# Kernel tuning notes

Measured on AMD Instinct MI355X. Metric: run time of the kernel, lower is better.

The kernel has to match this reference:

```python
import jax, jax.numpy as jnp
import numpy as np

E_DIM = 1024
HID = 4096
H = (2 * HID) // 3  # floor(2*hidden/3) = 2730
NUM_EXPERTS = 8
TOP_K = 2
LN_EPS = 1e-5


def setup_inputs() -> dict:
    key = jax.random.key(0)
    ks = jax.random.split(key, 10)
    B, T, P = 2, 8, 256
    s_in = 1.0 / np.sqrt(E_DIM)
    s_h = 1.0 / np.sqrt(H)
    return {
        "x": jax.random.normal(ks[0], (B, T, P, E_DIM), jnp.float32),
        "Wr": jax.random.normal(ks[1], (NUM_EXPERTS, E_DIM), jnp.float32) * s_in,
        "Wv": jax.random.normal(ks[2], (NUM_EXPERTS, E_DIM, H), jnp.float32) * s_in,
        "bv": jax.random.normal(ks[3], (NUM_EXPERTS, H), jnp.float32) * 0.01,
        "Wg": jax.random.normal(ks[4], (NUM_EXPERTS, E_DIM, H), jnp.float32) * s_in,
        "bg": jax.random.normal(ks[5], (NUM_EXPERTS, H), jnp.float32) * 0.01,
        "Wo": jax.random.normal(ks[6], (NUM_EXPERTS, H, E_DIM), jnp.float32) * s_h,
        "bo": jax.random.normal(ks[7], (NUM_EXPERTS, E_DIM), jnp.float32) * 0.01,
        "ln_g": jnp.ones((E_DIM,), jnp.float32),
        "ln_b": jnp.zeros((E_DIM,), jnp.float32),
    }


def reference(x, Wr, Wv, bv, Wg, bg, Wo, bo, ln_g, ln_b):
    B, T, P, E = x.shape
    flat = x.reshape(-1, E)          # [N, E]
    N = flat.shape[0]

    # router: top-k logits -> softmax combine weights
    logits = flat @ Wr.T                              # [N, C]
    tk_vals, tk_idx = jax.lax.top_k(logits, TOP_K)    # [N, K]
    tk_w = jax.nn.softmax(tk_vals, axis=-1)           # [N, K]

    # dense combine-weight matrix: zero for non-routed experts
    comb = jnp.zeros((N, NUM_EXPERTS), flat.dtype)
    comb = comb.at[jnp.arange(N)[:, None], tk_idx].add(tk_w)  # [N, C]

    # all experts over all tokens (masked combine makes this exact)
    hv = jnp.einsum('ne,ceh->cnh', flat, Wv) + bv[:, None, :]  # [C, N, H]
    hg = jnp.einsum('ne,ceh->cnh', flat, Wg) + bg[:, None, :]
    h = jax.nn.silu(hv) * hg                                   # SwiGLU
    oe = jnp.einsum('cnh,che->cne', h, Wo) + bo[:, None, :]    # [C, N, E]
    out = jnp.einsum('cne,nc->ne', oe, comb)                   # weighted combine

    # residual + LayerNorm (AdaptiveNormalizer with no conditioning)
    y = x + out.reshape(B, T, P, E)
    mu = jnp.mean(y, axis=-1, keepdims=True)
    var = jnp.mean((y - mu) ** 2, axis=-1, keepdims=True)
    return ln_g * (y - mu) * jax.lax.rsqrt(var + LN_EPS) + ln_b
```

## Files before the change

kernel.cpp:

```cpp
#include <hip/hip_runtime.h>
#include <hip/hip_bf16.h>

#define E_DIM 1024
#define HDIM  2730
#define HP    2752
#define NEXP  8
#define NTOK  4096
#define NPAIR 8192
#define LN_EPS 1e-5f

typedef __attribute__((ext_vector_type(8))) short  short8;
typedef __attribute__((ext_vector_type(4))) float  floatx4;
typedef __attribute__((ext_vector_type(4))) int    intx4;

__device__ __forceinline__ __hip_bfloat16 f2bf(float f) { return __float2bfloat16(f); }

__global__ __launch_bounds__(256) void router_k(const float* __restrict__ x,
    const float* __restrict__ Wr, int* __restrict__ counts,
    int* __restrict__ tk_idx, float* __restrict__ tk_w) {
  int wid = threadIdx.x >> 6, lane = threadIdx.x & 63;
  int t = blockIdx.x * 4 + wid;
  const float* xr = x + (size_t)t * E_DIM;
  float xv[16];
#pragma unroll
  for (int i = 0; i < 16; ++i) xv[i] = xr[lane + 64 * i];
  float lg[8];
#pragma unroll
  for (int e = 0; e < 8; ++e) {
    const float* wr = Wr + e * E_DIM;
    float a = 0.f;
#pragma unroll
    for (int i = 0; i < 16; ++i) a += xv[i] * wr[lane + 64 * i];
#pragma unroll
    for (int o = 32; o; o >>= 1) a += __shfl_xor(a, o, 64);
    lg[e] = a;
  }
  if (lane == 0) {
    int i0 = 0; float l0 = lg[0];
#pragma unroll
    for (int e = 1; e < 8; ++e) if (lg[e] > l0) { l0 = lg[e]; i0 = e; }
    int i1 = -1; float l1 = -1e30f;
#pragma unroll
    for (int e = 0; e < 8; ++e) if (e != i0 && lg[e] > l1) { l1 = lg[e]; i1 = e; }
    float w0 = 1.f / (1.f + __expf(l1 - l0));
    atomicAdd(&counts[i0], 1);
    atomicAdd(&counts[i1], 1);
    tk_idx[2 * t]     = i0;  tk_idx[2 * t + 1] = i1;
    tk_w[2 * t]       = w0;  tk_w[2 * t + 1]   = 1.f - w0;
  }
}

__global__ void offsets_k(const int* __restrict__ counts, int* __restrict__ offsets,
                          int* __restrict__ cursor) {
  if (threadIdx.x == 0) {
    int off = 0;
    for (int e = 0; e < NEXP; ++e) { offsets[e] = off; cursor[e] = off; off += counts[e]; }
  }
}

__global__ __launch_bounds__(256) void scatter_k(const int* __restrict__ tk_idx,
    const float* __restrict__ tk_w, int* __restrict__ cursor,
    int* __restrict__ pair_token, float* __restrict__ pair_w, int* __restrict__ pair_pos) {
  int t = blockIdx.x * 256 + threadIdx.x;
#pragma unroll
  for (int k = 0; k < 2; ++k) {
    int e = tk_idx[2 * t + k];
    int pos = atomicAdd(&cursor[e], 1);
    pair_token[pos] = t;
    pair_w[pos] = tk_w[2 * t + k];
    pair_pos[2 * t + k] = pos;
  }
}

__global__ __launch_bounds__(256) void xcvt_k(const float* __restrict__ x,
                                              __hip_bfloat16* __restrict__ xb) {
  size_t base = ((size_t)blockIdx.x * 256 + threadIdx.x) * 8;
  const floatx4* src = (const floatx4*)(x + base);
  floatx4 a = src[0], b = src[1];
  union { __hip_bfloat16 h[8]; intx4 v; } u;
#pragma unroll
  for (int j = 0; j < 4; ++j) { u.h[j] = f2bf(a[j]); u.h[4 + j] = f2bf(b[j]); }
  *(intx4*)(xb + base) = u.v;
}

__global__ __launch_bounds__(256) void tcvt_k(const float* __restrict__ in,
    __hip_bfloat16* __restrict__ out, int R, int C, int outRS,
    size_t inExpStride, size_t outExpStride) {
  __shared__ float tile[64 * 65];
  int e = blockIdx.z;
  const float* ip = in + inExpStride * e;
  __hip_bfloat16* op = out + outExpStride * e;
  int c0 = blockIdx.x * 64, r0 = blockIdx.y * 64;
#pragma unroll
  for (int i = 0; i < 16; ++i) {
    int idx = i * 256 + threadIdx.x;
    int rr = idx >> 6, cc = idx & 63;
    int gr = r0 + rr, gc = c0 + cc;
    tile[rr * 65 + cc] = (gr < R && gc < C) ? ip[(size_t)gr * C + gc] : 0.f;
  }
  __syncthreads();
#pragma unroll
  for (int i = 0; i < 16; ++i) {
    int idx = i * 256 + threadIdx.x;
    int cc = idx >> 6, rr = idx & 63;
    op[(size_t)(c0 + cc) * outRS + (r0 + rr)] = f2bf(tile[rr * 65 + cc]);
  }
}

template <bool PRE>
__global__ __launch_bounds__(256) void gemm1_k(
    const __hip_bfloat16* __restrict__ xb, const int* __restrict__ pair_token,
    const int* __restrict__ counts, const int* __restrict__ offsets,
    const float* __restrict__ Wv, const float* __restrict__ bv,
    const float* __restrict__ Wg, const float* __restrict__ bg,
    const __hip_bfloat16* __restrict__ WvT, const __hip_bfloat16* __restrict__ WgT,
    __hip_bfloat16* __restrict__ h) {
  int e = blockIdx.z;
  int Me = counts[e], off = offsets[e];
  int m0 = blockIdx.y * 128;
  if (m0 >= Me) return;
  int n0 = blockIdx.x * 64;

  __shared__ __hip_bfloat16 sA[128 * 40];
  __shared__ __hip_bfloat16 sBv[64 * 40];
  __shared__ __hip_bfloat16 sBg[64 * 40];
  __shared__ int sTok[128];

  int tid = threadIdx.x;
  if (tid < 128) {
    int m = m0 + tid;
    sTok[tid] = pair_token[off + (m < Me ? m : 0)];
  }
  __syncthreads();

  int wid = tid >> 6, lane = tid & 63;
  int wm = wid >> 1, wn = wid & 1;
  int q = lane >> 4, r = lane & 15;

  floatx4 accv[4][2], accg[4][2];
  floatx4 zz = {0.f, 0.f, 0.f, 0.f};
#pragma unroll
  for (int mi = 0; mi < 4; ++mi)
#pragma unroll
    for (int ni = 0; ni < 2; ++ni) { accv[mi][ni] = zz; accg[mi][ni] = zz; }

  for (int kt = 0; kt < E_DIM / 32; ++kt) {
    int k0 = kt * 32;
#pragma unroll
    for (int c = 0; c < 2; ++c) {
      int cid = c * 256 + tid;
      int m = cid >> 2, kk = (cid & 3) * 8;
      *(intx4*)(sA + m * 40 + kk) =
          *(const intx4*)(xb + (size_t)sTok[m] * E_DIM + k0 + kk);
    }
    if (PRE) {
      int nn = tid >> 2, kk = (tid & 3) * 8;
      size_t bbase = (size_t)e * ((size_t)HP * E_DIM) + (size_t)(n0 + nn) * E_DIM + k0 + kk;
      *(intx4*)(sBv + nn * 40 + kk) = *(const intx4*)(WvT + bbase);
      *(intx4*)(sBg + nn * 40 + kk) = *(const intx4*)(WgT + bbase);
    } else {
#pragma unroll
      for (int i = 0; i < 8; ++i) {
        int idx = i * 256 + tid;
        int kk = idx >> 6, nn = idx & 63;
        int n = n0 + nn;
        size_t gi = (size_t)e * E_DIM * HDIM + (size_t)(k0 + kk) * HDIM + n;
        float v = (n < HDIM) ? Wv[gi] : 0.f;
        float g = (n < HDIM) ? Wg[gi] : 0.f;
        sBv[nn * 40 + kk] = f2bf(v);
        sBg[nn * 40 + kk] = f2bf(g);
      }
    }
    __syncthreads();
    short8 av[4];
#pragma unroll
    for (int mi = 0; mi < 4; ++mi)
      av[mi] = *(const short8*)(sA + (wm * 64 + mi * 16 + r) * 40 + q * 8);
#pragma unroll
    for (int ni = 0; ni < 2; ++ni) {
      short8 b8v = *(const short8*)(sBv + (wn * 32 + ni * 16 + r) * 40 + q * 8);
      short8 b8g = *(const short8*)(sBg + (wn * 32 + ni * 16 + r) * 40 + q * 8);
#pragma unroll
      for (int mi = 0; mi < 4; ++mi) {
        accv[mi][ni] = __builtin_amdgcn_mfma_f32_16x16x32_bf16(av[mi], b8v, accv[mi][ni], 0, 0, 0);
        accg[mi][ni] = __builtin_amdgcn_mfma_f32_16x16x32_bf16(av[mi], b8g, accg[mi][ni], 0, 0, 0);
      }
    }
    __syncthreads();
  }

#pragma unroll
  for (int mi = 0; mi < 4; ++mi) {
#pragma unroll
    for (int rr = 0; rr < 4; ++rr) {
      int m_loc = wm * 64 + mi * 16 + q * 4 + rr;
      int m = m0 + m_loc;
      if (m >= Me) continue;
      size_t hrow = (size_t)(off + m) * HP;
#pragma unroll
      for (int ni = 0; ni < 2; ++ni) {
        int n = n0 + wn * 32 + ni * 16 + r;
        float bvv = (n < HDIM) ? bv[e * HDIM + n] : 0.f;
        float bgv = (n < HDIM) ? bg[e * HDIM + n] : 0.f;
        float hv = accv[mi][ni][rr] + bvv;
        float hg = accg[mi][ni][rr] + bgv;
        float s = 1.f / (1.f + __expf(-hv));
        h[hrow + n] = f2bf(hv * s * hg);
      }
    }
  }
}

template <bool PRE>
__global__ __launch_bounds__(256) void gemm2_k(
    const __hip_bfloat16* __restrict__ h,
    const int* __restrict__ counts, const int* __restrict__ offsets,
    const float* __restrict__ Wo, const float* __restrict__ bo,
    const __hip_bfloat16* __restrict__ WoT,
    float* __restrict__ pout) {
  int e = blockIdx.z;
  int Me = counts[e], off = offsets[e];
  int m0 = blockIdx.y * 128;
  if (m0 >= Me) return;
  int n0 = blockIdx.x * 64;

  __shared__ __hip_bfloat16 sA[128 * 40];
  __shared__ __hip_bfloat16 sB[64 * 40];

  int tid = threadIdx.x;
  int wid = tid >> 6, lane = tid & 63;
  int wm = wid >> 1, wn = wid & 1;
  int q = lane >> 4, r = lane & 15;

  floatx4 acc[4][2];
  floatx4 zz = {0.f, 0.f, 0.f, 0.f};
#pragma unroll
  for (int mi = 0; mi < 4; ++mi)
#pragma unroll
    for (int ni = 0; ni < 2; ++ni) acc[mi][ni] = zz;

  for (int kt = 0; kt < HP / 32; ++kt) {
    int k0 = kt * 32;
#pragma unroll
    for (int c = 0; c < 2; ++c) {
      int cid = c * 256 + tid;
      int m = cid >> 2, kk = (cid & 3) * 8;
      int row = off + m0 + m;
      if (row > NPAIR - 1) row = NPAIR - 1;
      *(intx4*)(sA + m * 40 + kk) = *(const intx4*)(h + (size_t)row * HP + k0 + kk);
    }
    if (PRE) {
      int nn = tid >> 2, kk = (tid & 3) * 8;
      *(intx4*)(sB + nn * 40 + kk) =
          *(const intx4*)(WoT + (size_t)e * ((size_t)E_DIM * HP) + (size_t)(n0 + nn) * HP + k0 + kk);
    } else {
#pragma unroll
      for (int i = 0; i < 8; ++i) {
        int idx = i * 256 + tid;
        int kk = idx >> 6, nn = idx & 63;
        int k = k0 + kk;
        float v = (k < HDIM) ? Wo[(size_t)e * HDIM * E_DIM + (size_t)k * E_DIM + n0 + nn] : 0.f;
        sB[nn * 40 + kk] = f2bf(v);
      }
    }
    __syncthreads();
    short8 av[4];
#pragma unroll
    for (int mi = 0; mi < 4; ++mi)
      av[mi] = *(const short8*)(sA + (wm * 64 + mi * 16 + r) * 40 + q * 8);
#pragma unroll
    for (int ni = 0; ni < 2; ++ni) {
      short8 b8 = *(const short8*)(sB + (wn * 32 + ni * 16 + r) * 40 + q * 8);
#pragma unroll
      for (int mi = 0; mi < 4; ++mi)
        acc[mi][ni] = __builtin_amdgcn_mfma_f32_16x16x32_bf16(av[mi], b8, acc[mi][ni], 0, 0, 0);
    }
    __syncthreads();
  }

#pragma unroll
  for (int mi = 0; mi < 4; ++mi) {
#pragma unroll
    for (int rr = 0; rr < 4; ++rr) {
      int m_loc = wm * 64 + mi * 16 + q * 4 + rr;
      int m = m0 + m_loc;
      if (m >= Me) continue;
      size_t orow = (size_t)(off + m) * E_DIM;
#pragma unroll
      for (int ni = 0; ni < 2; ++ni) {
        int n = n0 + wn * 32 + ni * 16 + r;
        pout[orow + n] = acc[mi][ni][rr] + bo[e * E_DIM + n];
      }
    }
  }
}

__global__ __launch_bounds__(256) void ln_k(const float* __restrict__ x,
    const float* __restrict__ pout, const int* __restrict__ pair_pos,
    const float* __restrict__ pair_w, const float* __restrict__ ln_g,
    const float* __restrict__ ln_b, float* __restrict__ out) {
  int t = blockIdx.x, tid = threadIdx.x;
  int p0 = pair_pos[2 * t], p1 = pair_pos[2 * t + 1];
  float w0 = pair_w[p0], w1 = pair_w[p1];
  const float* xr = x + (size_t)t * E_DIM;
  const float* r0 = pout + (size_t)p0 * E_DIM;
  const float* r1 = pout + (size_t)p1 * E_DIM;
  float y[4];
  float s = 0.f, ss = 0.f;
#pragma unroll
  for (int i = 0; i < 4; ++i) {
    int e = tid + 256 * i;
    y[i] = xr[e] + w0 * r0[e] + w1 * r1[e];
    s += y[i];
    ss += y[i] * y[i];
  }
#pragma unroll
  for (int o = 32; o; o >>= 1) { s += __shfl_xor(s, o, 64); ss += __shfl_xor(ss, o, 64); }
  __shared__ float red[8];
  int wid = tid >> 6, lane = tid & 63;
  if (lane == 0) { red[wid] = s; red[4 + wid] = ss; }
  __syncthreads();
  s  = red[0] + red[1] + red[2] + red[3];
  ss = red[4] + red[5] + red[6] + red[7];
  float mu = s * (1.f / E_DIM);
  float var = ss * (1.f / E_DIM) - mu * mu;
  float rs = rsqrtf(var + LN_EPS);
#pragma unroll
  for (int i = 0; i < 4; ++i) {
    int e = tid + 256 * i;
    out[(size_t)t * E_DIM + e] = ln_g[e] * (y[i] - mu) * rs + ln_b[e];
  }
}

extern "C" void kernel_launch(void* const* d_in, const int* in_sizes, int n_in,
                              void* d_out, int out_size, void* d_ws, size_t ws_size,
                              hipStream_t stream) {
  const float* x    = (const float*)d_in[0];
  const float* Wr   = (const float*)d_in[1];
  const float* Wv   = (const float*)d_in[2];
  const float* bv   = (const float*)d_in[3];
  const float* Wg   = (const float*)d_in[4];
  const float* bg   = (const float*)d_in[5];
  const float* Wo   = (const float*)d_in[6];
  const float* bo   = (const float*)d_in[7];
  const float* ln_g = (const float*)d_in[8];
  const float* ln_b = (const float*)d_in[9];
  float* out = (float*)d_out;

  char* ws = (char*)d_ws;
  size_t off = 0;
  auto alloc = [&](size_t bytes) -> void* {
    void* p = ws + off;
    off = (off + bytes + 255) & ~(size_t)255;
    return p;
  };
  int*   counts     = (int*)alloc(32);
  int*   cursor     = (int*)alloc(32);
  int*   offsets    = (int*)alloc(32);
  int*   tk_idx     = (int*)alloc((size_t)NTOK * 2 * 4);
  float* tk_w       = (float*)alloc((size_t)NTOK * 2 * 4);
  int*   pair_token = (int*)alloc((size_t)NPAIR * 4);
  float* pair_w     = (float*)alloc((size_t)NPAIR * 4);
  int*   pair_pos   = (int*)alloc((size_t)NPAIR * 4);
  __hip_bfloat16* xb   = (__hip_bfloat16*)alloc((size_t)NTOK * E_DIM * 2);
  __hip_bfloat16* hbuf = (__hip_bfloat16*)alloc((size_t)NPAIR * HP * 2);
  float* pout = (float*)alloc((size_t)NPAIR * E_DIM * 4);

  size_t welems = (size_t)NEXP * HP * E_DIM;
  size_t need_pre = off + 3 * (welems * 2 + 256);
  bool pre = (ws_size >= need_pre);
  __hip_bfloat16 *WvT = nullptr, *WgT = nullptr, *WoT = nullptr;
  if (pre) {
    WvT = (__hip_bfloat16*)alloc(welems * 2);
    WgT = (__hip_bfloat16*)alloc(welems * 2);
    WoT = (__hip_bfloat16*)alloc(welems * 2);
  }

  hipMemsetAsync(d_ws, 0, 768, stream);

  router_k<<<NTOK / 4, 256, 0, stream>>>(x, Wr, counts, tk_idx, tk_w);
  offsets_k<<<1, 64, 0, stream>>>(counts, offsets, cursor);
  scatter_k<<<NTOK / 256, 256, 0, stream>>>(tk_idx, tk_w, cursor, pair_token, pair_w, pair_pos);
  xcvt_k<<<(NTOK * E_DIM) / (256 * 8), 256, 0, stream>>>(x, xb);

  if (pre) {
    tcvt_k<<<dim3(HP / 64, E_DIM / 64, NEXP), 256, 0, stream>>>(
        Wv, WvT, E_DIM, HDIM, E_DIM, (size_t)E_DIM * HDIM, (size_t)HP * E_DIM);
    tcvt_k<<<dim3(HP / 64, E_DIM / 64, NEXP), 256, 0, stream>>>(
        Wg, WgT, E_DIM, HDIM, E_DIM, (size_t)E_DIM * HDIM, (size_t)HP * E_DIM);
    tcvt_k<<<dim3(E_DIM / 64, HP / 64, NEXP), 256, 0, stream>>>(
        Wo, WoT, HDIM, E_DIM, HP, (size_t)HDIM * E_DIM, (size_t)E_DIM * HP);
    gemm1_k<true><<<dim3(HP / 64, 32, NEXP), 256, 0, stream>>>(
        xb, pair_token, counts, offsets, Wv, bv, Wg, bg, WvT, WgT, hbuf);
    gemm2_k<true><<<dim3(E_DIM / 64, 32, NEXP), 256, 0, stream>>>(
        hbuf, counts, offsets, Wo, bo, WoT, pout);
  } else {
    gemm1_k<false><<<dim3(HP / 64, 32, NEXP), 256, 0, stream>>>(
        xb, pair_token, counts, offsets, Wv, bv, Wg, bg, nullptr, nullptr, hbuf);
    gemm2_k<false><<<dim3(E_DIM / 64, 32, NEXP), 256, 0, stream>>>(
        hbuf, counts, offsets, Wo, bo, nullptr, pout);
  }

  ln_k<<<NTOK, 256, 0, stream>>>(x, pout, pair_pos, pair_w, ln_g, ln_b, out);
}
```

Baseline: 784.1 us.

## Use direct global-to-LDS loads in expert GEMMs and vectorize weight transpose stores

The expert GEMM tiles are now loaded with global_load_lds 16-byte transfers straight into unpadded shared memory, which removes the per-thread register staging and LDS store instructions. The grid is swapped so blocks sharing a column tile of weights are adjacent in launch order, which may improve weight reuse in cache. The transpose-convert kernel now writes 8 bf16 values per 16-byte store, and the fallback non-pretransposed path is removed so the pre-transposed weights are always used. Dropping the padding may bring back LDS bank conflicts on the MFMA fragment reads, and the loop stays single-buffered with no overlap between loads and compute.

```diff
diff --git a/kernel.cpp b/kernel.cpp
--- a/kernel.cpp
+++ b/kernel.cpp
@@ -14,6 +14,11 @@
 typedef __attribute__((ext_vector_type(4))) int    intx4;
 
 __device__ __forceinline__ __hip_bfloat16 f2bf(float f) { return __float2bfloat16(f); }
+
+#define GLDS16(g, l)                                                        \
+  __builtin_amdgcn_global_load_lds(                                         \
+      (const __attribute__((address_space(1))) void*)(g),                   \
+      (__attribute__((address_space(3))) void*)(l), 16, 0, 0)
 
 __global__ __launch_bounds__(256) void router_k(const float* __restrict__ x,
     const float* __restrict__ Wr, int* __restrict__ counts,
@@ -100,36 +105,37 @@
   }
   __syncthreads();
 #pragma unroll
-  for (int i = 0; i < 16; ++i) {
+  for (int i = 0; i < 2; ++i) {
     int idx = i * 256 + threadIdx.x;
-    int cc = idx >> 6, rr = idx & 63;
-    op[(size_t)(c0 + cc) * outRS + (r0 + rr)] = f2bf(tile[rr * 65 + cc]);
-  }
-}
-
-template <bool PRE>
+    int cc = idx >> 3, rb = (idx & 7) * 8;
+    union { __hip_bfloat16 h[8]; intx4 v; } u;
+#pragma unroll
+    for (int j = 0; j < 8; ++j) u.h[j] = f2bf(tile[(rb + j) * 65 + cc]);
+    *(intx4*)(op + (size_t)(c0 + cc) * outRS + (r0 + rb)) = u.v;
+  }
+}
+
 __global__ __launch_bounds__(256) void gemm1_k(
     const __hip_bfloat16* __restrict__ xb, const int* __restrict__ pair_token,
     const int* __restrict__ counts, const int* __restrict__ offsets,
-    const float* __restrict__ Wv, const float* __restrict__ bv,
-    const float* __restrict__ Wg, const float* __restrict__ bg,
+    const float* __restrict__ bv, const float* __restrict__ bg,
     const __hip_bfloat16* __restrict__ WvT, const __hip_bfloat16* __restrict__ WgT,
     __hip_bfloat16* __restrict__ h) {
   int e = blockIdx.z;
   int Me = counts[e], off = offsets[e];
-  int m0 = blockIdx.y * 128;
+  int m0 = blockIdx.x * 128;
   if (m0 >= Me) return;
-  int n0 = blockIdx.x * 64;
-
-  __shared__ __hip_bfloat16 sA[128 * 40];
-  __shared__ __hip_bfloat16 sBv[64 * 40];
-  __shared__ __hip_bfloat16 sBg[64 * 40];
+  int n0 = blockIdx.y * 64;
+
+  __shared__ __hip_bfloat16 sA[128 * 32];
+  __shared__ __hip_bfloat16 sBv[64 * 32];
+  __shared__ __hip_bfloat16 sBg[64 * 32];
   __shared__ int sTok[128];
 
   int tid = threadIdx.x;
   if (tid < 128) {
     int m = m0 + tid;
-    sTok[tid] = pair_token[off + (m < Me ? m : 0)];
+    sTok[tid] = pair_token[off + (m < Me ? m : Me - 1)];
   }
   __syncthreads();
 
@@ -137,6 +143,19 @@
   int wm = wid >> 1, wn = wid & 1;
   int q = lane >> 4, r = lane & 15;
 
+  int lrow = lane >> 2, kl = (lane & 3) * 8;
+  int tok0 = sTok[wid * 32 + lrow];
+  int tok1 = sTok[wid * 32 + 16 + lrow];
+  const __hip_bfloat16* gA0 = xb + (size_t)tok0 * E_DIM + kl;
+  const __hip_bfloat16* gA1 = xb + (size_t)tok1 * E_DIM + kl;
+  size_t bbase = (size_t)e * ((size_t)HP * E_DIM) + (size_t)(n0 + wid * 16 + lrow) * E_DIM + kl;
+  const __hip_bfloat16* gBv = WvT + bbase;
+  const __hip_bfloat16* gBg = WgT + bbase;
+  __hip_bfloat16* dA0 = sA + (wid * 2 + 0) * 512;
+  __hip_bfloat16* dA1 = sA + (wid * 2 + 1) * 512;
+  __hip_bfloat16* dBv = sBv + wid * 512;
+  __hip_bfloat16* dBg = sBg + wid * 512;
+
   floatx4 accv[4][2], accg[4][2];
   floatx4 zz = {0.f, 0.f, 0.f, 0.f};
 #pragma unroll
@@ -145,41 +164,20 @@
     for (int ni = 0; ni < 2; ++ni) { accv[mi][ni] = zz; accg[mi][ni] = zz; }
 
   for (int kt = 0; kt < E_DIM / 32; ++kt) {
-    int k0 = kt * 32;
-#pragma unroll
-    for (int c = 0; c < 2; ++c) {
-      int cid = c * 256 + tid;
-      int m = cid >> 2, kk = (cid & 3) * 8;
-      *(intx4*)(sA + m * 40 + kk) =
-          *(const intx4*)(xb + (size_t)sTok[m] * E_DIM + k0 + kk);
-    }
-    if (PRE) {
-      int nn = tid >> 2, kk = (tid & 3) * 8;
-      size_t bbase = (size_t)e * ((size_t)HP * E_DIM) + (size_t)(n0 + nn) * E_DIM + k0 + kk;
-      *(intx4*)(sBv + nn * 40 + kk) = *(const intx4*)(WvT + bbase);
-      *(intx4*)(sBg + nn * 40 + kk) = *(const intx4*)(WgT + bbase);
-    } else {
-#pragma unroll
-      for (int i = 0; i < 8; ++i) {
-        int idx = i * 256 + tid;
-        int kk = idx >> 6, nn = idx & 63;
-        int n = n0 + nn;
-        size_t gi = (size_t)e * E_DIM * HDIM + (size_t)(k0 + kk) * HDIM + n;
-        float v = (n < HDIM) ? Wv[gi] : 0.f;
-        float g = (n < HDIM) ? Wg[gi] : 0.f;
-        sBv[nn * 40 + kk] = f2bf(v);
-        sBg[nn * 40 + kk] = f2bf(g);
-      }
-    }
+    GLDS16(gA0, dA0);
+    GLDS16(gA1, dA1);
+    GLDS16(gBv, dBv);
+    GLDS16(gBg, dBg);
+    gA0 += 32; gA1 += 32; gBv += 32; gBg += 32;
     __syncthreads();
     short8 av[4];
 #pragma unroll
     for (int mi = 0; mi < 4; ++mi)
-      av[mi] = *(const short8*)(sA + (wm * 64 + mi * 16 + r) * 40 + q * 8);
+      av[mi] = *(const short8*)(sA + (wm * 64 + mi * 16 + r) * 32 + q * 8);
 #pragma unroll
     for (int ni = 0; ni < 2; ++ni) {
-      short8 b8v = *(const short8*)(sBv + (wn * 32 + ni * 16 + r) * 40 + q * 8);
-      short8 b8g = *(const short8*)(sBg + (wn * 32 + ni * 16 + r) * 40 + q * 8);
+      short8 b8v = *(const short8*)(sBv + (wn * 32 + ni * 16 + r) * 32 + q * 8);
+      short8 b8g = *(const short8*)(sBg + (wn * 32 + ni * 16 + r) * 32 + q * 8);
 #pragma unroll
       for (int mi = 0; mi < 4; ++mi) {
         accv[mi][ni] = __builtin_amdgcn_mfma_f32_16x16x32_bf16(av[mi], b8v, accv[mi][ni], 0, 0, 0);
@@ -211,27 +209,35 @@
   }
 }
 
-template <bool PRE>
 __global__ __launch_bounds__(256) void gemm2_k(
     const __hip_bfloat16* __restrict__ h,
     const int* __restrict__ counts, const int* __restrict__ offsets,
-    const float* __restrict__ Wo, const float* __restrict__ bo,
+    const float* __restrict__ bo,
     const __hip_bfloat16* __restrict__ WoT,
     float* __restrict__ pout) {
   int e = blockIdx.z;
   int Me = counts[e], off = offsets[e];
-  int m0 = blockIdx.y * 128;
+  int m0 = blockIdx.x * 128;
   if (m0 >= Me) return;
-  int n0 = blockIdx.x * 64;
-
-  __shared__ __hip_bfloat16 sA[128 * 40];
-  __shared__ __hip_bfloat16 sB[64 * 40];
+  int n0 = blockIdx.y * 64;
+
+  __shared__ __hip_bfloat16 sA[128 * 32];
+  __shared__ __hip_bfloat16 sB[64 * 32];
 
   int tid = threadIdx.x;
   int wid = tid >> 6, lane = tid & 63;
   int wm = wid >> 1, wn = wid & 1;
   int q = lane >> 4, r = lane & 15;
 
+  int lrow = lane >> 2, kl = (lane & 3) * 8;
+  const __hip_bfloat16* gA0 = h + (size_t)(off + m0 + wid * 32 + lrow) * HP + kl;
+  const __hip_bfloat16* gA1 = h + (size_t)(off + m0 + wid * 32 + 16 + lrow) * HP + kl;
+  const __hip_bfloat16* gB =
+      WoT + (size_t)e * ((size_t)E_DIM * HP) + (size_t)(n0 + wid * 16 + lrow) * HP + kl;
+  __hip_bfloat16* dA0 = sA + (wid * 2 + 0) * 512;
+  __hip_bfloat16* dA1 = sA + (wid * 2 + 1) * 512;
+  __hip_bfloat16* dB = sB + wid * 512;
+
   floatx4 acc[4][2];
   floatx4 zz = {0.f, 0.f, 0.f, 0.f};
 #pragma unroll
@@ -240,37 +246,18 @@
     for (int ni = 0; ni < 2; ++ni) acc[mi][ni] = zz;
 
   for (int kt = 0; kt < HP / 32; ++kt) {
-    int k0 = kt * 32;
-#pragma unroll
-    for (int c = 0; c < 2; ++c) {
-      int cid = c * 256 + tid;
-      int m = cid >> 2, kk = (cid & 3) * 8;
-      int row = off + m0 + m;
-      if (row > NPAIR - 1) row = NPAIR - 1;
-      *(intx4*)(sA + m * 40 + kk) = *(const intx4*)(h + (size_t)row * HP + k0 + kk);
-    }
-    if (PRE) {
-      int nn = tid >> 2, kk = (tid & 3) * 8;
-      *(intx4*)(sB + nn * 40 + kk) =
-          *(const intx4*)(WoT + (size_t)e * ((size_t)E_DIM * HP) + (size_t)(n0 + nn) * HP + k0 + kk);
-    } else {
-#pragma unroll
-      for (int i = 0; i < 8; ++i) {
-        int idx = i * 256 + tid;
-        int kk = idx >> 6, nn = idx & 63;
-        int k = k0 + kk;
-        float v = (k < HDIM) ? Wo[(size_t)e * HDIM * E_DIM + (size_t)k * E_DIM + n0 + nn] : 0.f;
-        sB[nn * 40 + kk] = f2bf(v);
-      }
-    }
+    GLDS16(gA0, dA0);
+    GLDS16(gA1, dA1);
+    GLDS16(gB, dB);
+    gA0 += 32; gA1 += 32; gB += 32;
     __syncthreads();
     short8 av[4];
 #pragma unroll
     for (int mi = 0; mi < 4; ++mi)
-      av[mi] = *(const short8*)(sA + (wm * 64 + mi * 16 + r) * 40 + q * 8);
+      av[mi] = *(const short8*)(sA + (wm * 64 + mi * 16 + r) * 32 + q * 8);
 #pragma unroll
     for (int ni = 0; ni < 2; ++ni) {
-      short8 b8 = *(const short8*)(sB + (wn * 32 + ni * 16 + r) * 40 + q * 8);
+      short8 b8 = *(const short8*)(sB + (wn * 32 + ni * 16 + r) * 32 + q * 8);
 #pragma unroll
       for (int mi = 0; mi < 4; ++mi)
         acc[mi][ni] = __builtin_amdgcn_mfma_f32_16x16x32_bf16(av[mi], b8, acc[mi][ni], 0, 0, 0);
@@ -367,14 +354,9 @@
   float* pout = (float*)alloc((size_t)NPAIR * E_DIM * 4);
 
   size_t welems = (size_t)NEXP * HP * E_DIM;
-  size_t need_pre = off + 3 * (welems * 2 + 256);
-  bool pre = (ws_size >= need_pre);
-  __hip_bfloat16 *WvT = nullptr, *WgT = nullptr, *WoT = nullptr;
-  if (pre) {
-    WvT = (__hip_bfloat16*)alloc(welems * 2);
-    WgT = (__hip_bfloat16*)alloc(welems * 2);
-    WoT = (__hip_bfloat16*)alloc(welems * 2);
-  }
+  __hip_bfloat16* WvT = (__hip_bfloat16*)alloc(welems * 2);
+  __hip_bfloat16* WgT = (__hip_bfloat16*)alloc(welems * 2);
+  __hip_bfloat16* WoT = (__hip_bfloat16*)alloc(welems * 2);
 
   hipMemsetAsync(d_ws, 0, 768, stream);
 
@@ -383,23 +365,17 @@
   scatter_k<<<NTOK / 256, 256, 0, stream>>>(tk_idx, tk_w, cursor, pair_token, pair_w, pair_pos);
   xcvt_k<<<(NTOK * E_DIM) / (256 * 8), 256, 0, stream>>>(x, xb);
 
-  if (pre) {
-    tcvt_k<<<dim3(HP / 64, E_DIM / 64, NEXP), 256, 0, stream>>>(
-        Wv, WvT, E_DIM, HDIM, E_DIM, (size_t)E_DIM * HDIM, (size_t)HP * E_DIM);
-    tcvt_k<<<dim3(HP / 64, E_DIM / 64, NEXP), 256, 0, stream>>>(
-        Wg, WgT, E_DIM, HDIM, E_DIM, (size_t)E_DIM * HDIM, (size_t)HP * E_DIM);
-    tcvt_k<<<dim3(E_DIM / 64, HP / 64, NEXP), 256, 0, stream>>>(
-        Wo, WoT, HDIM, E_DIM, HP, (size_t)HDIM * E_DIM, (size_t)E_DIM * HP);
-    gemm1_k<true><<<dim3(HP / 64, 32, NEXP), 256, 0, stream>>>(
-        xb, pair_token, counts, offsets, Wv, bv, Wg, bg, WvT, WgT, hbuf);
-    gemm2_k<true><<<dim3(E_DIM / 64, 32, NEXP), 256, 0, stream>>>(
-        hbuf, counts, offsets, Wo, bo, WoT, pout);
-  } else {
-    gemm1_k<false><<<dim3(HP / 64, 32, NEXP), 256, 0, stream>>>(
-        xb, pair_token, counts, offsets, Wv, bv, Wg, bg, nullptr, nullptr, hbuf);
-    gemm2_k<false><<<dim3(E_DIM / 64, 32, NEXP), 256, 0, stream>>>(
-        hbuf, counts, offsets, Wo, bo, nullptr, pout);
-  }
+  tcvt_k<<<dim3(HP / 64, E_DIM / 64, NEXP), 256, 0, stream>>>(
+      Wv, WvT, E_DIM, HDIM, E_DIM, (size_t)E_DIM * HDIM, (size_t)HP * E_DIM);
+  tcvt_k<<<dim3(HP / 64, E_DIM / 64, NEXP), 256, 0, stream>>>(
+      Wg, WgT, E_DIM, HDIM, E_DIM, (size_t)E_DIM * HDIM, (size_t)HP * E_DIM);
+  tcvt_k<<<dim3(E_DIM / 64, HP / 64, NEXP), 256, 0, stream>>>(
+      Wo, WoT, HDIM, E_DIM, HP, (size_t)HDIM * E_DIM, (size_t)E_DIM * HP);
+
+  gemm1_k<<<dim3(32, HP / 64, NEXP), 256, 0, stream>>>(
+      xb, pair_token, counts, offsets, bv, bg, WvT, WgT, hbuf);
+  gemm2_k<<<dim3(32, E_DIM / 64, NEXP), 256, 0, stream>>>(
+      hbuf, counts, offsets, bo, WoT, pout);
 
   ln_k<<<NTOK, 256, 0, stream>>>(x, pout, pair_pos, pair_w, ln_g, ln_b, out);
 }
```

Result: slower. 1.195 ms (+52.4%).
